# Kernel tuning notes

Hardware: AMD Instinct MI355X
Metric: run time of the kernel (lower is better)

## Reference

```python
import jax, jax.numpy as jnp
import numpy as np

B, T, F = 4096, 72, 9
H = 64            # GRU units per direction
DENSE = 128
P = 24            # predict_window


def _gru_scan(xp, h0, U, br, act):
    """xp: (T,B,3H) precomputed input projections; Keras reset_after=True GRU."""
    def step(h, x_t):
        rec = h @ U + br                      # (B,3H)
        xz, xr, xh = jnp.split(x_t, 3, axis=-1)
        rz, rr, rh = jnp.split(rec, 3, axis=-1)
        z = jax.nn.sigmoid(xz + rz)
        r = jax.nn.sigmoid(xr + rr)
        hh = act(xh + r * rh)
        h_new = z * h + (1.0 - z) * hh
        return h_new, h_new
    hT, hs = jax.lax.scan(step, h0, xp)
    return hT, hs


def _bigru(x, h0f, h0b, Wf, Uf, bif, brf, Wb, Ub, bib, brb, act, return_sequences):
    xt = jnp.swapaxes(x, 0, 1)                # (T,B,F)
    xpf = xt @ Wf + bif                       # (T,B,3H)
    xpb = xt[::-1] @ Wb + bib                 # reversed time for backward dir
    hTf, hsf = _gru_scan(xpf, h0f, Uf, brf, act)
    hTb, hsb = _gru_scan(xpb, h0b, Ub, brb, act)
    if return_sequences:
        out = jnp.concatenate([hsf, hsb[::-1]], axis=-1)   # (T,B,2H)
        return jnp.swapaxes(out, 0, 1)                      # (B,T,2H)
    return jnp.concatenate([hTf, hTb], axis=-1)             # (B,2H)


def _glorot(key, shape):
    fan_in, fan_out = shape[0], shape[-1]
    lim = np.sqrt(6.0 / (fan_in + fan_out))
    return jax.random.uniform(key, shape, jnp.float32, -lim, lim)


def setup_inputs() -> dict:
    key = jax.random.key(0)
    ks = jax.random.split(key, 16)
    d = {
        "x": jax.random.normal(ks[0], (B, T, F), jnp.float32),
        "h0_fwd": jnp.zeros((B, H), jnp.float32),
        "h0_bwd": jnp.zeros((B, H), jnp.float32),
        # d1 (input F=9), forward & backward directions
        "d1f_W": _glorot(ks[1], (F, 3 * H)), "d1f_U": _glorot(ks[2], (H, 3 * H)),
        "d1f_bi": jnp.zeros((3 * H,), jnp.float32), "d1f_br": jnp.zeros((3 * H,), jnp.float32),
        "d1b_W": _glorot(ks[3], (F, 3 * H)), "d1b_U": _glorot(ks[4], (H, 3 * H)),
        "d1b_bi": jnp.zeros((3 * H,), jnp.float32), "d1b_br": jnp.zeros((3 * H,), jnp.float32),
        # d2 (input 2H=128)
        "d2f_W": _glorot(ks[5], (2 * H, 3 * H)), "d2f_U": _glorot(ks[6], (H, 3 * H)),
        "d2f_bi": jnp.zeros((3 * H,), jnp.float32), "d2f_br": jnp.zeros((3 * H,), jnp.float32),
        "d2b_W": _glorot(ks[7], (2 * H, 3 * H)), "d2b_U": _glorot(ks[8], (H, 3 * H)),
        "d2b_bi": jnp.zeros((3 * H,), jnp.float32), "d2b_br": jnp.zeros((3 * H,), jnp.float32),
        # dense heads
        "dense_W": _glorot(ks[9], (2 * H, DENSE)), "dense_b": jnp.zeros((DENSE,), jnp.float32),
        "out_W": _glorot(ks[10], (DENSE, P)), "out_b": jnp.zeros((P,), jnp.float32),
    }
    return d


def reference(x, h0_fwd, h0_bwd,
              d1f_W, d1f_U, d1f_bi, d1f_br, d1b_W, d1b_U, d1b_bi, d1b_br,
              d2f_W, d2f_U, d2f_bi, d2f_br, d2b_W, d2b_U, d2b_bi, d2b_br,
              dense_W, dense_b, out_W, out_b):
    # d1: Bidirectional GRU(64, activation=relu), return_sequences=True, initial_state=hidden
    seq = _bigru(x, h0_fwd, h0_bwd,
                 d1f_W, d1f_U, d1f_bi, d1f_br,
                 d1b_W, d1b_U, d1b_bi, d1b_br,
                 jax.nn.relu, True)                         # (B,T,128)
    # d2: Bidirectional GRU(64, activation=tanh), zero initial state, last-state output
    z0 = jnp.zeros((x.shape[0], H), seq.dtype)
    feat = _bigru(seq, z0, z0,
                  d2f_W, d2f_U, d2f_bi, d2f_br,
                  d2b_W, d2b_U, d2b_bi, d2b_br,
                  jnp.tanh, False)                          # (B,128)
    h = jax.nn.relu(feat @ dense_W + dense_b)               # (B,128)
    out = jax.nn.softmax(h @ out_W + out_b, axis=-1)        # (B,P)
    return out
```

## Files before the change

### kernel.cpp

```cpp
#include <hip/hip_runtime.h>
#include <hip/hip_bf16.h>

typedef __attribute__((ext_vector_type(8))) short short8;
typedef __attribute__((ext_vector_type(4))) float f32x4;

#define MFMA_B16(a, b, c) __builtin_amdgcn_mfma_f32_16x16x32_bf16((a), (b), (c), 0, 0, 0)

__device__ __forceinline__ float bf2f(unsigned short u) {
    union { unsigned int i; float f; } v; v.i = ((unsigned int)u) << 16; return v.f;
}
__device__ __forceinline__ unsigned short f2bf(float f) {
    union { float f; unsigned int i; } v; v.f = f;
    unsigned int r = v.i + 0x7fffu + ((v.i >> 16) & 1u);
    return (unsigned short)(r >> 16);
}
__device__ __forceinline__ float rcp_f(float x) { return __builtin_amdgcn_rcpf(x); }
__device__ __forceinline__ float sigm_pre(float x) {
    return rcp_f(1.0f + __builtin_amdgcn_exp2f(x));
}
__device__ __forceinline__ float tanh_pre(float x) {
    return 1.0f - 2.0f * rcp_f(__builtin_amdgcn_exp2f(x) + 1.0f);
}

__device__ __forceinline__ bool probe_bf16(const unsigned short* p, int tid, int* s_cnt) {
    if (tid == 0) *s_cnt = 0;
    __syncthreads();
    unsigned short s = p[tid & 255];
    int e = (s >> 7) & 0xFF;
    if (tid < 256 && e >= 117 && e <= 137) atomicAdd(s_cnt, 1);
    __syncthreads();
    return *s_cnt >= 200;
}

struct WArgs {
    const void* src[20];
    int off[21];
};

__global__ __launch_bounds__(256)
void convert_w(WArgs a, unsigned short* __restrict__ arena,
               const unsigned short* __restrict__ probe)
{
    __shared__ int cnt;
    const bool bf = probe_bf16(probe, threadIdx.x, &cnt);
    const int total = a.off[20];
    for (int i = blockIdx.x * 256 + threadIdx.x; i < total; i += gridDim.x * 256) {
        int t = 0;
        while (t < 19 && i >= a.off[t + 1]) ++t;
        const int local = i - a.off[t];
        float v = bf ? bf2f(((const unsigned short*)a.src[t])[local])
                     : ((const float*)a.src[t])[local];
        if (t < 16) {
            const int col = local % 192;
            if (col < 128) v *= -1.4426950408889634f;
            else if (t >= 8) v *= 2.885390081777927f;
        }
        arena[i] = f2bf(v);
    }
}

__global__ __launch_bounds__(256, 1)
void gru1_kernel(const void* __restrict__ X, const void* __restrict__ h0f,
                 const void* __restrict__ h0b, int cb, int bchunk,
                 const unsigned short* __restrict__ Wf, const unsigned short* __restrict__ Uf,
                 const unsigned short* __restrict__ bif, const unsigned short* __restrict__ brf,
                 const unsigned short* __restrict__ Wb, const unsigned short* __restrict__ Ub,
                 const unsigned short* __restrict__ bib, const unsigned short* __restrict__ brb,
                 unsigned short* __restrict__ seq)
{
    const int tid  = threadIdx.x;
    const int lane = tid & 63;
    const int wv   = tid >> 6;
    const int q    = lane >> 4;
    const int ln   = lane & 15;
    const int dir  = blockIdx.y;
    const int lb0  = blockIdx.x * 16;
    const int gb0  = cb + lb0;
    const int u    = wv * 16 + ln;

    const unsigned short* W  = dir ? Wb  : Wf;
    const unsigned short* U  = dir ? Ub  : Uf;
    const unsigned short* bi = dir ? bib : bif;
    const unsigned short* br = dir ? brb : brf;
    const void* h0 = dir ? h0b : h0f;

    __shared__ __align__(16) unsigned short Ah[2][16][72];
    __shared__ __align__(16) unsigned short Ax[2][16][40];
    __shared__ int s_cnt;

    const bool xbf = probe_bf16((const unsigned short*)X, tid, &s_cnt);

    {
        unsigned short* p = &Ax[0][0][0];
        for (int i = tid; i < 2 * 16 * 40; i += 256) p[i] = 0;
    }
    __syncthreads();

    {
        const int tx0 = dir ? 71 : 0;
        if (tid < 144) {
            int r = tid / 9, k = tid - 9 * r;
            size_t idx = ((size_t)(gb0 + r) * 72 + tx0) * 9 + k;
            unsigned short hv, lv;
            if (xbf) { hv = ((const unsigned short*)X)[idx]; lv = 0; }
            else { float v = ((const float*)X)[idx]; hv = f2bf(v); lv = f2bf(v - bf2f(hv)); }
            Ax[0][r][2 * k]     = hv;
            Ax[0][r][2 * k + 1] = lv;
        }
    }

    short8 bU[3][2];
    short8 bW[3];
#pragma unroll
    for (int g = 0; g < 3; ++g) {
        const int col = g * 64 + u;
#pragma unroll
        for (int ks = 0; ks < 2; ++ks) {
            short8 f;
#pragma unroll
            for (int j = 0; j < 8; ++j) {
                int kp = ks * 32 + q * 8 + j;
                f[j] = (short)U[(size_t)kp * 192 + col];
            }
            bU[g][ks] = f;
        }
        short8 fw;
#pragma unroll
        for (int j = 0; j < 8; ++j) {
            int kp = q * 8 + j;
            fw[j] = (kp < 18) ? (short)W[(size_t)(kp >> 1) * 192 + col] : (short)0;
        }
        bW[g] = fw;
    }

    const float bz  = bf2f(bi[u])       + bf2f(br[u]);
    const float brg = bf2f(bi[64 + u])  + bf2f(br[64 + u]);
    const float bih = bf2f(bi[128 + u]);
    const float brh = bf2f(br[128 + u]);
    const f32x4 Cz  = {bz,  bz,  bz,  bz};
    const f32x4 Cr  = {brg, brg, brg, brg};
    const f32x4 Chx = {bih, bih, bih, bih};
    const f32x4 Chr = {brh, brh, brh, brh};

    float hreg[4];
#pragma unroll
    for (int i = 0; i < 4; ++i) {
        int m = q * 4 + i;
        size_t idx = (size_t)(gb0 + m) * 64 + u;
        float hv = xbf ? bf2f(((const unsigned short*)h0)[idx])
                       : ((const float*)h0)[idx];
        hreg[i] = hv;
        Ah[0][m][u] = f2bf(hv);
    }

    const int r2 = tid >> 3, c2 = tid & 7;
    const int r0x = tid / 9, k0x = tid - 9 * r0x;

    unsigned short ch = 0, cl = 0;
    if (tid < 144) {
        const int tx = dir ? 70 : 1;
        size_t idx = ((size_t)(gb0 + r0x) * 72 + tx) * 9 + k0x;
        if (xbf) { ch = ((const unsigned short*)X)[idx]; cl = 0; }
        else { float v = ((const float*)X)[idx]; ch = f2bf(v); cl = f2bf(v - bf2f(ch)); }
    }
    __syncthreads();

#pragma unroll 2
    for (int t = 0; t < 72; ++t) {
        const int cur = t & 1, nb = cur ^ 1;

        unsigned short fh = 0, fl = 0;
        if (t < 70 && tid < 144) {
            const int tx = dir ? (69 - t) : (t + 2);
            size_t idx = ((size_t)(gb0 + r0x) * 72 + tx) * 9 + k0x;
            if (xbf) { fh = ((const unsigned short*)X)[idx]; fl = 0; }
            else { float v = ((const float*)X)[idx]; fh = f2bf(v); fl = f2bf(v - bf2f(fh)); }
        }

        if (t > 0 && tid < 128) {
            const int tw = dir ? (71 - (t - 1)) : (t - 1);
            int4 v = *(const int4*)&Ah[cur][r2][c2 * 8];
            *(int4*)(seq + ((size_t)tw * bchunk + lb0 + r2) * 128 + dir * 64 + c2 * 8) = v;
        }

        const unsigned short* ap = &Ah[cur][ln][0];
        short8 a0 = *(const short8*)(ap + q * 8);
        short8 a1 = *(const short8*)(ap + 32 + q * 8);
        short8 ax = *(const short8*)(&Ax[cur][ln][q * 8]);
        f32x4 az  = MFMA_B16(ax, bW[0], Cz);
        az        = MFMA_B16(a0, bU[0][0], az);
        az        = MFMA_B16(a1, bU[0][1], az);
        f32x4 ar  = MFMA_B16(ax, bW[1], Cr);
        ar        = MFMA_B16(a0, bU[1][0], ar);
        ar        = MFMA_B16(a1, bU[1][1], ar);
        f32x4 ahx = MFMA_B16(ax, bW[2], Chx);
        f32x4 ahr = MFMA_B16(a0, bU[2][0], Chr);
        ahr       = MFMA_B16(a1, bU[2][1], ahr);

#pragma unroll
        for (int i = 0; i < 4; ++i) {
            const int m = q * 4 + i;
            float z = sigm_pre(az[i]);
            float r = sigm_pre(ar[i]);
            float pre = ahx[i] + r * ahr[i];
            float hh = fmaxf(pre, 0.0f);
            float hn = hh + z * (hreg[i] - hh);
            hreg[i] = hn;
            Ah[nb][m][u] = f2bf(hn);
        }

        if (t < 71 && tid < 144) {
            Ax[nb][r0x][2 * k0x]     = ch;
            Ax[nb][r0x][2 * k0x + 1] = cl;
        }
        ch = fh; cl = fl;
        __syncthreads();
    }

    if (tid < 128) {
        const int tw = dir ? 0 : 71;
        int4 v = *(const int4*)&Ah[0][r2][c2 * 8];
        *(int4*)(seq + ((size_t)tw * bchunk + lb0 + r2) * 128 + dir * 64 + c2 * 8) = v;
    }
}

__global__ __launch_bounds__(256, 1)
void gru2_kernel(const unsigned short* __restrict__ seq, int cb, int bchunk,
                 const unsigned short* __restrict__ W2f, const unsigned short* __restrict__ U2f,
                 const unsigned short* __restrict__ bi2f, const unsigned short* __restrict__ br2f,
                 const unsigned short* __restrict__ W2b, const unsigned short* __restrict__ U2b,
                 const unsigned short* __restrict__ bi2b, const unsigned short* __restrict__ br2b,
                 float* __restrict__ feat)
{
    const int tid  = threadIdx.x;
    const int lane = tid & 63;
    const int wv   = tid >> 6;
    const int q    = lane >> 4;
    const int ln   = lane & 15;
    const int dir  = blockIdx.y;
    const int lb0  = blockIdx.x * 16;
    const int gb0  = cb + lb0;
    const int u    = wv * 16 + ln;

    const unsigned short* W  = dir ? W2b  : W2f;
    const unsigned short* U  = dir ? U2b  : U2f;
    const unsigned short* bi = dir ? bi2b : bi2f;
    const unsigned short* br = dir ? br2b : br2f;

    __shared__ __align__(16) unsigned short Ah[2][16][72];

    {
        unsigned short* p = &Ah[0][0][0];
        for (int i = tid; i < 16 * 72; i += 256) p[i] = 0;
    }

    const long long tstride = (long long)bchunk * 128 * (dir ? -1 : 1);
    const unsigned short* sptr0 = seq + ((size_t)(lb0 + ln)) * 128 + q * 8
                                + (dir ? 71ll * bchunk * 128 : 0);

    short8 bU[3][2];
    short8 bV[3][4];
#pragma unroll
    for (int g = 0; g < 3; ++g) {
        const int col = g * 64 + u;
#pragma unroll
        for (int ks = 0; ks < 2; ++ks) {
            short8 f;
#pragma unroll
            for (int j = 0; j < 8; ++j) {
                int kp = ks * 32 + q * 8 + j;
                f[j] = (short)U[(size_t)kp * 192 + col];
            }
            bU[g][ks] = f;
        }
#pragma unroll
        for (int ks = 0; ks < 4; ++ks) {
            short8 fv;
#pragma unroll
            for (int j = 0; j < 8; ++j) {
                int kp = ks * 32 + q * 8 + j;
                fv[j] = (short)W[(size_t)kp * 192 + col];
            }
            bV[g][ks] = fv;
        }
    }

    const float bz  = bf2f(bi[u])       + bf2f(br[u]);
    const float brg = bf2f(bi[64 + u])  + bf2f(br[64 + u]);
    const float bih = bf2f(bi[128 + u]);
    const float brh = bf2f(br[128 + u]);
    const f32x4 Cz  = {bz,  bz,  bz,  bz};
    const f32x4 Cr  = {brg, brg, brg, brg};
    const f32x4 Chx = {bih, bih, bih, bih};
    const f32x4 Chr = {brh, brh, brh, brh};

    float hreg[4];
#pragma unroll
    for (int i = 0; i < 4; ++i) hreg[i] = 0.0f;

    f32x4 P0, P1, P2;
    {
        const unsigned short* sp = sptr0;
        short8 s0 = *(const short8*)(sp);
        short8 s1 = *(const short8*)(sp + 32);
        short8 s2 = *(const short8*)(sp + 64);
        short8 s3 = *(const short8*)(sp + 96);
        P0 = MFMA_B16(s0, bV[0][0], Cz);
        P0 = MFMA_B16(s1, bV[0][1], P0);
        P0 = MFMA_B16(s2, bV[0][2], P0);
        P0 = MFMA_B16(s3, bV[0][3], P0);
        P1 = MFMA_B16(s0, bV[1][0], Cr);
        P1 = MFMA_B16(s1, bV[1][1], P1);
        P1 = MFMA_B16(s2, bV[1][2], P1);
        P1 = MFMA_B16(s3, bV[1][3], P1);
        P2 = MFMA_B16(s0, bV[2][0], Chx);
        P2 = MFMA_B16(s1, bV[2][1], P2);
        P2 = MFMA_B16(s2, bV[2][2], P2);
        P2 = MFMA_B16(s3, bV[2][3], P2);
    }
    short8 c0, c1, c2, c3;
    {
        const unsigned short* sp = sptr0 + tstride;
        c0 = *(const short8*)(sp);
        c1 = *(const short8*)(sp + 32);
        c2 = *(const short8*)(sp + 64);
        c3 = *(const short8*)(sp + 96);
    }
    __syncthreads();

#pragma unroll 2
    for (int t = 0; t < 72; ++t) {
        const int cur = t & 1, nb = cur ^ 1;

        short8 f0, f1, f2, f3;
        const bool pf2 = (t < 70);
        if (pf2) {
            const unsigned short* sp = sptr0 + (long long)(t + 2) * tstride;
            f0 = *(const short8*)(sp);
            f1 = *(const short8*)(sp + 32);
            f2 = *(const short8*)(sp + 64);
            f3 = *(const short8*)(sp + 96);
        }

        const unsigned short* ap = &Ah[cur][ln][0];
        short8 a0 = *(const short8*)(ap + q * 8);
        short8 a1 = *(const short8*)(ap + 32 + q * 8);
        f32x4 az  = MFMA_B16(a0, bU[0][0], P0);
        az        = MFMA_B16(a1, bU[0][1], az);
        f32x4 ar  = MFMA_B16(a0, bU[1][0], P1);
        ar        = MFMA_B16(a1, bU[1][1], ar);
        f32x4 ahr = MFMA_B16(a0, bU[2][0], Chr);
        ahr       = MFMA_B16(a1, bU[2][1], ahr);
        f32x4 ahx = P2;

#pragma unroll
        for (int i = 0; i < 4; ++i) {
            const int m = q * 4 + i;
            float z = sigm_pre(az[i]);
            float r = sigm_pre(ar[i]);
            float pre = ahx[i] + r * ahr[i];
            float hh = tanh_pre(pre);
            float hn = hh + z * (hreg[i] - hh);
            hreg[i] = hn;
            Ah[nb][m][u] = f2bf(hn);
        }

        if (t < 71) {
            P0 = MFMA_B16(c0, bV[0][0], Cz);
            P0 = MFMA_B16(c1, bV[0][1], P0);
            P0 = MFMA_B16(c2, bV[0][2], P0);
            P0 = MFMA_B16(c3, bV[0][3], P0);
            P1 = MFMA_B16(c0, bV[1][0], Cr);
            P1 = MFMA_B16(c1, bV[1][1], P1);
            P1 = MFMA_B16(c2, bV[1][2], P1);
            P1 = MFMA_B16(c3, bV[1][3], P1);
            P2 = MFMA_B16(c0, bV[2][0], Chx);
            P2 = MFMA_B16(c1, bV[2][1], P2);
            P2 = MFMA_B16(c2, bV[2][2], P2);
            P2 = MFMA_B16(c3, bV[2][3], P2);
        }
        if (pf2) { c0 = f0; c1 = f1; c2 = f2; c3 = f3; }
        __syncthreads();
    }

#pragma unroll
    for (int i = 0; i < 4; ++i) {
        const int m = q * 4 + i;
        feat[(size_t)(gb0 + m) * 128 + dir * 64 + u] = hreg[i];
    }
}

__global__ __launch_bounds__(256, 1)
void head_kernel(const float* __restrict__ feat,
                 const unsigned short* __restrict__ dW, const unsigned short* __restrict__ db,
                 const unsigned short* __restrict__ oW, const unsigned short* __restrict__ ob,
                 float* __restrict__ out)
{
    const int tid = threadIdx.x;
    const int b0  = blockIdx.x * 16;

    __shared__ __align__(16) unsigned short Wl[128][136];
    __shared__ __align__(16) float fs[16][128];
    __shared__ __align__(16) float hs[16][136];
    __shared__ __align__(16) float ls[16][32];

    for (int i = tid; i < 2048; i += 256) {
        const int k = i >> 4;
        const int c = (i & 15) * 8;
        *(int4*)&Wl[k][c] = *(const int4*)(dW + (size_t)k * 128 + c);
    }
    {
        const float4* src = (const float4*)(feat + (size_t)b0 * 128);
        float4* dst = (float4*)&fs[0][0];
        for (int i = tid; i < 512; i += 256) dst[i] = src[i];
    }
    __syncthreads();

    {
        const int row = tid >> 4;
        const int j0  = (tid & 15) * 8;
        float acc[8];
#pragma unroll
        for (int jj = 0; jj < 8; ++jj) acc[jj] = bf2f(db[j0 + jj]);
        for (int k = 0; k < 128; ++k) {
            float f = fs[row][k];
            short8 w = *(const short8*)&Wl[k][j0];
#pragma unroll
            for (int jj = 0; jj < 8; ++jj)
                acc[jj] += f * bf2f((unsigned short)w[jj]);
        }
#pragma unroll
        for (int jj = 0; jj < 8; ++jj) hs[row][j0 + jj] = fmaxf(acc[jj], 0.0f);
    }
    __syncthreads();

    for (int e = tid; e < 16 * 24; e += 256) {
        const int row = e / 24, l = e - 24 * row;
        float acc = bf2f(ob[l]);
        for (int k = 0; k < 128; ++k)
            acc += hs[row][k] * bf2f(oW[(size_t)k * 24 + l]);
        ls[row][l] = acc;
    }
    __syncthreads();

    for (int e = tid; e < 16 * 24; e += 256) {
        const int row = e / 24, l = e - 24 * row;
        float mx = ls[row][0];
#pragma unroll
        for (int k = 1; k < 24; ++k) mx = fmaxf(mx, ls[row][k]);
        float s = 0.0f;
#pragma unroll
        for (int k = 0; k < 24; ++k) s += __expf(ls[row][k] - mx);
        float v = __expf(ls[row][l] - mx) * rcp_f(s);
        out[(size_t)(b0 + row) * 24 + l] = v;
    }
}

extern "C" void kernel_launch(void* const* d_in, const int* in_sizes, int n_in,
                              void* d_out, int out_size, void* d_ws, size_t ws_size,
                              hipStream_t stream) {
    (void)in_sizes; (void)n_in; (void)out_size;

    static const int wc[20] = {
        1728, 12288, 192, 192,
        1728, 12288, 192, 192,
        24576, 12288, 192, 192,
        24576, 12288, 192, 192,
        16384, 128,
        3072, 24
    };

    WArgs a;
    int off = 0;
    for (int t = 0; t < 20; ++t) {
        a.src[t] = d_in[t + 3];
        a.off[t] = off;
        off += wc[t];
    }
    a.off[20] = off;

    const unsigned long long arena_bytes = 245952ull;
    const unsigned long long feat_bytes  = 4096ull * 128ull * 4ull;
    const unsigned long long seq_full    = 72ull * 4096ull * 128ull * 2ull;
    const unsigned long long fixed       = arena_bytes + feat_bytes;

    int nc = 32;
    for (int c = 1; c <= 32; c *= 2) {
        if (fixed + seq_full / (unsigned long long)c <= (unsigned long long)ws_size) { nc = c; break; }
    }
    const int bchunk = 4096 / nc;

    unsigned short* arena = (unsigned short*)d_ws;
    float* feat           = (float*)((char*)d_ws + arena_bytes);
    unsigned short* seq   = (unsigned short*)((char*)d_ws + fixed);

    convert_w<<<128, 256, 0, stream>>>(a, arena, (const unsigned short*)d_in[0]);

    const unsigned short* d1fW = arena + a.off[0];
    const unsigned short* d1fU = arena + a.off[1];
    const unsigned short* d1fbi= arena + a.off[2];
    const unsigned short* d1fbr= arena + a.off[3];
    const unsigned short* d1bW = arena + a.off[4];
    const unsigned short* d1bU = arena + a.off[5];
    const unsigned short* d1bbi= arena + a.off[6];
    const unsigned short* d1bbr= arena + a.off[7];
    const unsigned short* d2fW = arena + a.off[8];
    const unsigned short* d2fU = arena + a.off[9];
    const unsigned short* d2fbi= arena + a.off[10];
    const unsigned short* d2fbr= arena + a.off[11];
    const unsigned short* d2bW = arena + a.off[12];
    const unsigned short* d2bU = arena + a.off[13];
    const unsigned short* d2bbi= arena + a.off[14];
    const unsigned short* d2bbr= arena + a.off[15];
    const unsigned short* dW   = arena + a.off[16];
    const unsigned short* db   = arena + a.off[17];
    const unsigned short* oW   = arena + a.off[18];
    const unsigned short* ob   = arena + a.off[19];

    for (int c = 0; c < nc; ++c) {
        const int cb = c * bchunk;
        gru1_kernel<<<dim3(bchunk / 16, 2), 256, 0, stream>>>(
            d_in[0], d_in[1], d_in[2], cb, bchunk,
            d1fW, d1fU, d1fbi, d1fbr, d1bW, d1bU, d1bbi, d1bbr, seq);
        gru2_kernel<<<dim3(bchunk / 16, 2), 256, 0, stream>>>(
            seq, cb, bchunk,
            d2fW, d2fU, d2fbi, d2fbr, d2bW, d2bU, d2bbi, d2bbr, feat);
    }
    head_kernel<<<256, 256, 0, stream>>>(
        feat, dW, db, oW, ob, (float*)d_out);
}
```

Before: 256.3 us.

## Run each GRU direction tile in one wavefront and split gru2 into producer/consumer waves

gru1 now runs on a single 64-lane wave per 16-row tile, with each lane computing all 64 hidden units through four MFMA column tiles. This removes the per-step block barriers and the LDS staging of x, which is now loaded with vector reads and converted in registers. gru2 uses two waves: a producer computes input projections and a consumer runs the recurrence, synchronised by lightweight LDS barriers. The cost is far higher register pressure per lane and fewer threads per block, which may lower occupancy or cause spills.

```diff
diff --git a/kernel.cpp b/kernel.cpp
--- a/kernel.cpp
+++ b/kernel.cpp
@@ -3,31 +3,51 @@
 
 typedef __attribute__((ext_vector_type(8))) short short8;
 typedef __attribute__((ext_vector_type(4))) float f32x4;
+typedef float float4a __attribute__((ext_vector_type(4), aligned(4)));
+typedef unsigned short ushort4u __attribute__((ext_vector_type(4), aligned(2)));
+typedef unsigned short ush;
 
 #define MFMA_B16(a, b, c) __builtin_amdgcn_mfma_f32_16x16x32_bf16((a), (b), (c), 0, 0, 0)
 
-__device__ __forceinline__ float bf2f(unsigned short u) {
+__device__ __forceinline__ float bf2f(ush u) {
     union { unsigned int i; float f; } v; v.i = ((unsigned int)u) << 16; return v.f;
 }
-__device__ __forceinline__ unsigned short f2bf(float f) {
+__device__ __forceinline__ ush f2bf(float f) {
     union { float f; unsigned int i; } v; v.f = f;
     unsigned int r = v.i + 0x7fffu + ((v.i >> 16) & 1u);
-    return (unsigned short)(r >> 16);
+    return (ush)(r >> 16);
 }
 __device__ __forceinline__ float rcp_f(float x) { return __builtin_amdgcn_rcpf(x); }
 __device__ __forceinline__ float sigm_pre(float x) {
     return rcp_f(1.0f + __builtin_amdgcn_exp2f(x));
 }
-__device__ __forceinline__ float tanh_pre(float x) {
-    return 1.0f - 2.0f * rcp_f(__builtin_amdgcn_exp2f(x) + 1.0f);
-}
-
-__device__ __forceinline__ bool probe_bf16(const unsigned short* p, int tid, int* s_cnt) {
+
+__device__ __forceinline__ void lds_barrier() {
+    asm volatile("s_waitcnt lgkmcnt(0)" ::: "memory");
+    __builtin_amdgcn_s_barrier();
+    asm volatile("" ::: "memory");
+}
+
+__device__ __forceinline__ bool probe_bf16(const ush* p, int tid, int* s_cnt) {
     if (tid == 0) *s_cnt = 0;
     __syncthreads();
-    unsigned short s = p[tid & 255];
+    ush s = p[tid & 255];
     int e = (s >> 7) & 0xFF;
     if (tid < 256 && e >= 117 && e <= 137) atomicAdd(s_cnt, 1);
+    __syncthreads();
+    return *s_cnt >= 200;
+}
+__device__ __forceinline__ bool probe_bf16_64(const ush* p, int lane, int* s_cnt) {
+    if (lane == 0) *s_cnt = 0;
+    __syncthreads();
+    int c = 0;
+#pragma unroll
+    for (int k = 0; k < 4; ++k) {
+        ush s = p[lane * 4 + k];
+        int e = (s >> 7) & 0xFF;
+        c += (e >= 117 && e <= 137) ? 1 : 0;
+    }
+    atomicAdd(s_cnt, c);
     __syncthreads();
     return *s_cnt >= 200;
 }
@@ -38,8 +58,7 @@
 };
 
 __global__ __launch_bounds__(256)
-void convert_w(WArgs a, unsigned short* __restrict__ arena,
-               const unsigned short* __restrict__ probe)
+void convert_w(WArgs a, ush* __restrict__ arena, const ush* __restrict__ probe)
 {
     __shared__ int cnt;
     const bool bf = probe_bf16(probe, threadIdx.x, &cnt);
@@ -48,7 +67,7 @@
         int t = 0;
         while (t < 19 && i >= a.off[t + 1]) ++t;
         const int local = i - a.off[t];
-        float v = bf ? bf2f(((const unsigned short*)a.src[t])[local])
+        float v = bf ? bf2f(((const ush*)a.src[t])[local])
                      : ((const float*)a.src[t])[local];
         if (t < 16) {
             const int col = local % 192;
@@ -59,347 +78,386 @@
     }
 }
 
-__global__ __launch_bounds__(256, 1)
+struct XR { float4a f; ushort4u h; };
+
+__device__ __forceinline__ XR loadx(const void* X, bool xbf, size_t row72, int tx, int q) {
+    XR r;
+    r.f = (float4a){0.f, 0.f, 0.f, 0.f};
+    r.h = (ushort4u){0, 0, 0, 0};
+    if (xbf) {
+        const ush* p = (const ush*)X + (row72 + (size_t)tx) * 9 + q * 4;
+        if (q < 2) r.h = *(const ushort4u*)p;
+        else if (q == 2) r.h[0] = p[0];
+    } else {
+        const float* p = (const float*)X + (row72 + (size_t)tx) * 9 + q * 4;
+        if (q < 2) r.f = *(const float4a*)p;
+        else if (q == 2) r.f[0] = p[0];
+    }
+    return r;
+}
+
+__device__ __forceinline__ short8 convx(bool xbf, float4a rf, ushort4u rh) {
+    short8 r;
+    if (xbf) {
+#pragma unroll
+        for (int j = 0; j < 4; ++j) { r[2 * j] = (short)rh[j]; r[2 * j + 1] = 0; }
+    } else {
+#pragma unroll
+        for (int j = 0; j < 4; ++j) {
+            ush hi = f2bf(rf[j]);
+            ush lo = f2bf(rf[j] - bf2f(hi));
+            r[2 * j] = (short)hi; r[2 * j + 1] = (short)lo;
+        }
+    }
+    return r;
+}
+
+#define GRU1_STEP(T, AX, RFO, RHO)                                              \
+    do {                                                                        \
+        const short8 axu_ = AX;                            \
+        if ((T) < 70) AX = convx(xbf, RFO, RHO);          \
+        if ((T) < 68) {                                                         \
+            XR rr = loadx(X, xbf, row72, dir ? 67 - (T) : (T) + 4, q);          \
+            RFO = rr.f; RHO = rr.h;                                             \
+        }                                                                       \
+        short8 a0 = *(const short8*)&Ah[ln][q * 8];                             \
+        short8 a1 = *(const short8*)&Ah[ln][32 + q * 8];                        \
+        if ((T) > 0) {                                                          \
+            const int tw = dir ? 71 - ((T) - 1) : (T) - 1;                      \
+            ush* sp = seq + ((size_t)tw * bchunk + lb0 + ln) * 128 + dir * 64;  \
+            *(short8*)(sp + q * 8) = a0;                                        \
+            *(short8*)(sp + 32 + q * 8) = a1;                                   \
+        }                                                                       \
+        f32x4 az[4], ar[4], ahx[4], ahr[4];                                     \
+        _Pragma("unroll") for (int n = 0; n < 4; ++n) {                         \
+            az[n]  = MFMA_B16(axu_, bW[0][n], Cz[n]);                           \
+            az[n]  = MFMA_B16(a0, bU[0][0][n], az[n]);                          \
+            az[n]  = MFMA_B16(a1, bU[0][1][n], az[n]);                          \
+            ar[n]  = MFMA_B16(axu_, bW[1][n], Cr[n]);                           \
+            ar[n]  = MFMA_B16(a0, bU[1][0][n], ar[n]);                          \
+            ar[n]  = MFMA_B16(a1, bU[1][1][n], ar[n]);                          \
+            ahx[n] = MFMA_B16(axu_, bW[2][n], Chx[n]);                          \
+            ahr[n] = MFMA_B16(a0, bU[2][0][n], Chr[n]);                         \
+            ahr[n] = MFMA_B16(a1, bU[2][1][n], ahr[n]);                         \
+        }                                                                       \
+        _Pragma("unroll") for (int n = 0; n < 4; ++n)                           \
+            _Pragma("unroll") for (int i = 0; i < 4; ++i) {                     \
+                float z = sigm_pre(az[n][i]);                                   \
+                float r = sigm_pre(ar[n][i]);                                   \
+                float pre = ahx[n][i] + r * ahr[n][i];                          \
+                float hh = fmaxf(pre, 0.0f);                                    \
+                float hn = hh + z * (hreg[n][i] - hh);                          \
+                hreg[n][i] = hn;                                                \
+                Ah[q * 4 + i][n * 16 + ln] = f2bf(hn);                          \
+            }                                                                   \
+    } while (0)
+
+__global__ __launch_bounds__(64, 1)
 void gru1_kernel(const void* __restrict__ X, const void* __restrict__ h0f,
                  const void* __restrict__ h0b, int cb, int bchunk,
-                 const unsigned short* __restrict__ Wf, const unsigned short* __restrict__ Uf,
-                 const unsigned short* __restrict__ bif, const unsigned short* __restrict__ brf,
-                 const unsigned short* __restrict__ Wb, const unsigned short* __restrict__ Ub,
-                 const unsigned short* __restrict__ bib, const unsigned short* __restrict__ brb,
-                 unsigned short* __restrict__ seq)
+                 const ush* __restrict__ Wf, const ush* __restrict__ Uf,
+                 const ush* __restrict__ bif, const ush* __restrict__ brf,
+                 const ush* __restrict__ Wb, const ush* __restrict__ Ub,
+                 const ush* __restrict__ bib, const ush* __restrict__ brb,
+                 ush* __restrict__ seq)
 {
-    const int tid  = threadIdx.x;
-    const int lane = tid & 63;
-    const int wv   = tid >> 6;
-    const int q    = lane >> 4;
-    const int ln   = lane & 15;
-    const int dir  = blockIdx.y;
-    const int lb0  = blockIdx.x * 16;
-    const int gb0  = cb + lb0;
-    const int u    = wv * 16 + ln;
-
-    const unsigned short* W  = dir ? Wb  : Wf;
-    const unsigned short* U  = dir ? Ub  : Uf;
-    const unsigned short* bi = dir ? bib : bif;
-    const unsigned short* br = dir ? brb : brf;
+    const int lane = threadIdx.x & 63;
+    const int q = lane >> 4, ln = lane & 15;
+    const int dir = blockIdx.y;
+    const int lb0 = blockIdx.x * 16;
+    const int gb0 = cb + lb0;
+
+    const ush* W  = dir ? Wb  : Wf;
+    const ush* U  = dir ? Ub  : Uf;
+    const ush* bi = dir ? bib : bif;
+    const ush* br = dir ? brb : brf;
     const void* h0 = dir ? h0b : h0f;
 
-    __shared__ __align__(16) unsigned short Ah[2][16][72];
-    __shared__ __align__(16) unsigned short Ax[2][16][40];
+    __shared__ __align__(16) ush Ah[16][72];
     __shared__ int s_cnt;
 
-    const bool xbf = probe_bf16((const unsigned short*)X, tid, &s_cnt);
+    const bool xbf = probe_bf16_64((const ush*)X, lane, &s_cnt);
+
+    short8 bU[3][2][4];
+    short8 bW[3][4];
+#pragma unroll
+    for (int g = 0; g < 3; ++g)
+#pragma unroll
+        for (int n = 0; n < 4; ++n) {
+            const int col = g * 64 + n * 16 + ln;
+#pragma unroll
+            for (int ks = 0; ks < 2; ++ks) {
+                short8 f;
+#pragma unroll
+                for (int j = 0; j < 8; ++j) {
+                    int kp = ks * 32 + q * 8 + j;
+                    f[j] = (short)U[(size_t)kp * 192 + col];
+                }
+                bU[g][ks][n] = f;
+            }
+            short8 fw;
+#pragma unroll
+            for (int j = 0; j < 8; ++j) {
+                int kp = q * 8 + j;
+                fw[j] = (kp < 18) ? (short)W[(size_t)(kp >> 1) * 192 + col] : (short)0;
+            }
+            bW[g][n] = fw;
+        }
+
+    f32x4 Cz[4], Cr[4], Chx[4], Chr[4];
+#pragma unroll
+    for (int n = 0; n < 4; ++n) {
+        const int u2 = n * 16 + ln;
+        const float bz  = bf2f(bi[u2]) + bf2f(br[u2]);
+        const float brg = bf2f(bi[64 + u2]) + bf2f(br[64 + u2]);
+        const float bih = bf2f(bi[128 + u2]);
+        const float brh = bf2f(br[128 + u2]);
+        Cz[n]  = (f32x4){bz, bz, bz, bz};
+        Cr[n]  = (f32x4){brg, brg, brg, brg};
+        Chx[n] = (f32x4){bih, bih, bih, bih};
+        Chr[n] = (f32x4){brh, brh, brh, brh};
+    }
+
+    float hreg[4][4];
+#pragma unroll
+    for (int n = 0; n < 4; ++n)
+#pragma unroll
+        for (int i = 0; i < 4; ++i) {
+            size_t idx = (size_t)(gb0 + q * 4 + i) * 64 + n * 16 + ln;
+            float hv = xbf ? bf2f(((const ush*)h0)[idx]) : ((const float*)h0)[idx];
+            hreg[n][i] = hv;
+            Ah[q * 4 + i][n * 16 + ln] = f2bf(hv);
+        }
+
+    const size_t row72 = (size_t)(gb0 + ln) * 72;
+    XR r0 = loadx(X, xbf, row72, dir ? 71 : 0, q);
+    XR r1 = loadx(X, xbf, row72, dir ? 70 : 1, q);
+    XR r2 = loadx(X, xbf, row72, dir ? 69 : 2, q);
+    XR r3 = loadx(X, xbf, row72, dir ? 68 : 3, q);
+    short8 ax0 = convx(xbf, r0.f, r0.h);
+    short8 ax1 = convx(xbf, r1.f, r1.h);
+    float4a rf0 = r2.f; ushort4u rh0 = r2.h;
+    float4a rf1 = r3.f; ushort4u rh1 = r3.h;
+
+    for (int t = 0; t < 72; t += 2) {
+        GRU1_STEP(t,     ax0, rf0, rh0);
+        GRU1_STEP(t + 1, ax1, rf1, rh1);
+    }
 
     {
-        unsigned short* p = &Ax[0][0][0];
-        for (int i = tid; i < 2 * 16 * 40; i += 256) p[i] = 0;
-    }
-    __syncthreads();
-
-    {
-        const int tx0 = dir ? 71 : 0;
-        if (tid < 144) {
-            int r = tid / 9, k = tid - 9 * r;
-            size_t idx = ((size_t)(gb0 + r) * 72 + tx0) * 9 + k;
-            unsigned short hv, lv;
-            if (xbf) { hv = ((const unsigned short*)X)[idx]; lv = 0; }
-            else { float v = ((const float*)X)[idx]; hv = f2bf(v); lv = f2bf(v - bf2f(hv)); }
-            Ax[0][r][2 * k]     = hv;
-            Ax[0][r][2 * k + 1] = lv;
-        }
-    }
-
-    short8 bU[3][2];
-    short8 bW[3];
-#pragma unroll
-    for (int g = 0; g < 3; ++g) {
-        const int col = g * 64 + u;
-#pragma unroll
-        for (int ks = 0; ks < 2; ++ks) {
-            short8 f;
-#pragma unroll
-            for (int j = 0; j < 8; ++j) {
-                int kp = ks * 32 + q * 8 + j;
-                f[j] = (short)U[(size_t)kp * 192 + col];
-            }
-            bU[g][ks] = f;
-        }
-        short8 fw;
-#pragma unroll
-        for (int j = 0; j < 8; ++j) {
-            int kp = q * 8 + j;
-            fw[j] = (kp < 18) ? (short)W[(size_t)(kp >> 1) * 192 + col] : (short)0;
-        }
-        bW[g] = fw;
-    }
-
-    const float bz  = bf2f(bi[u])       + bf2f(br[u]);
-    const float brg = bf2f(bi[64 + u])  + bf2f(br[64 + u]);
-    const float bih = bf2f(bi[128 + u]);
-    const float brh = bf2f(br[128 + u]);
-    const f32x4 Cz  = {bz,  bz,  bz,  bz};
-    const f32x4 Cr  = {brg, brg, brg, brg};
-    const f32x4 Chx = {bih, bih, bih, bih};
-    const f32x4 Chr = {brh, brh, brh, brh};
-
-    float hreg[4];
-#pragma unroll
-    for (int i = 0; i < 4; ++i) {
-        int m = q * 4 + i;
-        size_t idx = (size_t)(gb0 + m) * 64 + u;
-        float hv = xbf ? bf2f(((const unsigned short*)h0)[idx])
-                       : ((const float*)h0)[idx];
-        hreg[i] = hv;
-        Ah[0][m][u] = f2bf(hv);
-    }
-
-    const int r2 = tid >> 3, c2 = tid & 7;
-    const int r0x = tid / 9, k0x = tid - 9 * r0x;
-
-    unsigned short ch = 0, cl = 0;
-    if (tid < 144) {
-        const int tx = dir ? 70 : 1;
-        size_t idx = ((size_t)(gb0 + r0x) * 72 + tx) * 9 + k0x;
-        if (xbf) { ch = ((const unsigned short*)X)[idx]; cl = 0; }
-        else { float v = ((const float*)X)[idx]; ch = f2bf(v); cl = f2bf(v - bf2f(ch)); }
-    }
-    __syncthreads();
-
-#pragma unroll 2
-    for (int t = 0; t < 72; ++t) {
-        const int cur = t & 1, nb = cur ^ 1;
-
-        unsigned short fh = 0, fl = 0;
-        if (t < 70 && tid < 144) {
-            const int tx = dir ? (69 - t) : (t + 2);
-            size_t idx = ((size_t)(gb0 + r0x) * 72 + tx) * 9 + k0x;
-            if (xbf) { fh = ((const unsigned short*)X)[idx]; fl = 0; }
-            else { float v = ((const float*)X)[idx]; fh = f2bf(v); fl = f2bf(v - bf2f(fh)); }
-        }
-
-        if (t > 0 && tid < 128) {
-            const int tw = dir ? (71 - (t - 1)) : (t - 1);
-            int4 v = *(const int4*)&Ah[cur][r2][c2 * 8];
-            *(int4*)(seq + ((size_t)tw * bchunk + lb0 + r2) * 128 + dir * 64 + c2 * 8) = v;
-        }
-
-        const unsigned short* ap = &Ah[cur][ln][0];
-        short8 a0 = *(const short8*)(ap + q * 8);
-        short8 a1 = *(const short8*)(ap + 32 + q * 8);
-        short8 ax = *(const short8*)(&Ax[cur][ln][q * 8]);
-        f32x4 az  = MFMA_B16(ax, bW[0], Cz);
-        az        = MFMA_B16(a0, bU[0][0], az);
-        az        = MFMA_B16(a1, bU[0][1], az);
-        f32x4 ar  = MFMA_B16(ax, bW[1], Cr);
-        ar        = MFMA_B16(a0, bU[1][0], ar);
-        ar        = MFMA_B16(a1, bU[1][1], ar);
-        f32x4 ahx = MFMA_B16(ax, bW[2], Chx);
-        f32x4 ahr = MFMA_B16(a0, bU[2][0], Chr);
-        ahr       = MFMA_B16(a1, bU[2][1], ahr);
-
-#pragma unroll
-        for (int i = 0; i < 4; ++i) {
-            const int m = q * 4 + i;
-            float z = sigm_pre(az[i]);
-            float r = sigm_pre(ar[i]);
-            float pre = ahx[i] + r * ahr[i];
-            float hh = fmaxf(pre, 0.0f);
-            float hn = hh + z * (hreg[i] - hh);
-            hreg[i] = hn;
-            Ah[nb][m][u] = f2bf(hn);
-        }
-
-        if (t < 71 && tid < 144) {
-            Ax[nb][r0x][2 * k0x]     = ch;
-            Ax[nb][r0x][2 * k0x + 1] = cl;
-        }
-        ch = fh; cl = fl;
-        __syncthreads();
-    }
-
-    if (tid < 128) {
+        short8 a0 = *(const short8*)&Ah[ln][q * 8];
+        short8 a1 = *(const short8*)&Ah[ln][32 + q * 8];
         const int tw = dir ? 0 : 71;
-        int4 v = *(const int4*)&Ah[0][r2][c2 * 8];
-        *(int4*)(seq + ((size_t)tw * bchunk + lb0 + r2) * 128 + dir * 64 + c2 * 8) = v;
-    }
-}
-
-__global__ __launch_bounds__(256, 1)
-void gru2_kernel(const unsigned short* __restrict__ seq, int cb, int bchunk,
-                 const unsigned short* __restrict__ W2f, const unsigned short* __restrict__ U2f,
-                 const unsigned short* __restrict__ bi2f, const unsigned short* __restrict__ br2f,
-                 const unsigned short* __restrict__ W2b, const unsigned short* __restrict__ U2b,
-                 const unsigned short* __restrict__ bi2b, const unsigned short* __restrict__ br2b,
+        ush* sp = seq + ((size_t)tw * bchunk + lb0 + ln) * 128 + dir * 64;
+        *(short8*)(sp + q * 8) = a0;
+        *(short8*)(sp + 32 + q * 8) = a1;
+    }
+}
+
+#define PROD_STEP(FA, BUFI, T)                                                 \
+    do {                                                                       \
+        if ((T) < 71) {                                                        \
+            _Pragma("unroll") for (int g = 0; g < 3; ++g) {                    \
+                _Pragma("unroll") for (int n = 0; n < 4; ++n) {                \
+                    f32x4 acc = MFMA_B16(FA[0], bV[g][0][n], Cg[g][n]);        \
+                    acc = MFMA_B16(FA[1], bV[g][1][n], acc);                   \
+                    acc = MFMA_B16(FA[2], bV[g][2][n], acc);                   \
+                    acc = MFMA_B16(FA[3], bV[g][3][n], acc);                   \
+                    *(f32x4*)&Pbuf[BUFI][g][n][poff] = acc;                    \
+                }                                                              \
+            }                                                                  \
+        }                                                                      \
+        if ((T) < 69) {                                                        \
+            const ush* sp = sptr0 + (long long)((T) + 3) * tstride;            \
+            FA[0] = *(const short8*)sp;                                        \
+            FA[1] = *(const short8*)(sp + 32);                                 \
+            FA[2] = *(const short8*)(sp + 64);                                 \
+            FA[3] = *(const short8*)(sp + 96);                                 \
+        }                                                                      \
+    } while (0)
+
+#define CONS_STEP(BUFI, T)                                                     \
+    do {                                                                       \
+        f32x4 Pz[4], Pr[4], Pc[4];                                             \
+        _Pragma("unroll") for (int n = 0; n < 4; ++n) {                        \
+            Pz[n] = *(const f32x4*)&Pbuf[BUFI][0][n][poff];                    \
+            Pr[n] = *(const f32x4*)&Pbuf[BUFI][1][n][poff];                    \
+            Pc[n] = *(const f32x4*)&Pbuf[BUFI][2][n][poff];                    \
+        }                                                                      \
+        short8 a0 = *(const short8*)&Ah[ln][q * 8];                            \
+        short8 a1 = *(const short8*)&Ah[ln][32 + q * 8];                       \
+        f32x4 az[4], ar[4], ahr[4];                                            \
+        _Pragma("unroll") for (int n = 0; n < 4; ++n) {                        \
+            az[n]  = MFMA_B16(a0, bU[0][0][n], Pz[n]);                         \
+            az[n]  = MFMA_B16(a1, bU[0][1][n], az[n]);                         \
+            ar[n]  = MFMA_B16(a0, bU[1][0][n], Pr[n]);                         \
+            ar[n]  = MFMA_B16(a1, bU[1][1][n], ar[n]);                         \
+            ahr[n] = MFMA_B16(a0, bU[2][0][n], Chr[n]);                        \
+            ahr[n] = MFMA_B16(a1, bU[2][1][n], ahr[n]);                        \
+        }                                                                      \
+        _Pragma("unroll") for (int n = 0; n < 4; ++n)                          \
+            _Pragma("unroll") for (int i = 0; i < 4; ++i) {                    \
+                float z = sigm_pre(az[n][i]);                                  \
+                float r = sigm_pre(ar[n][i]);                                  \
+                float pre = Pc[n][i] + r * ahr[n][i];                          \
+                float e = __builtin_amdgcn_exp2f(pre);         \
+                float hh = 1.0f - 2.0f * rcp_f(e + 1.0f);                      \
+                float hn = hh + z * (hreg[n][i] - hh);                         \
+                hreg[n][i] = hn;                                               \
+                Ah[q * 4 + i][n * 16 + ln] = f2bf(hn);                         \
+            }                                                                  \
+    } while (0)
+
+__global__ __launch_bounds__(128, 1)
+void gru2_kernel(const ush* __restrict__ seq, int cb, int bchunk,
+                 const ush* __restrict__ W2f, const ush* __restrict__ U2f,
+                 const ush* __restrict__ bi2f, const ush* __restrict__ br2f,
+                 const ush* __restrict__ W2b, const ush* __restrict__ U2b,
+                 const ush* __restrict__ bi2b, const ush* __restrict__ br2b,
                  float* __restrict__ feat)
 {
-    const int tid  = threadIdx.x;
-    const int lane = tid & 63;
-    const int wv   = tid >> 6;
-    const int q    = lane >> 4;
-    const int ln   = lane & 15;
-    const int dir  = blockIdx.y;
-    const int lb0  = blockIdx.x * 16;
-    const int gb0  = cb + lb0;
-    const int u    = wv * 16 + ln;
-
-    const unsigned short* W  = dir ? W2b  : W2f;
-    const unsigned short* U  = dir ? U2b  : U2f;
-    const unsigned short* bi = dir ? bi2b : bi2f;
-    const unsigned short* br = dir ? br2b : br2f;
-
-    __shared__ __align__(16) unsigned short Ah[2][16][72];
-
-    {
-        unsigned short* p = &Ah[0][0][0];
-        for (int i = tid; i < 16 * 72; i += 256) p[i] = 0;
-    }
-
-    const long long tstride = (long long)bchunk * 128 * (dir ? -1 : 1);
-    const unsigned short* sptr0 = seq + ((size_t)(lb0 + ln)) * 128 + q * 8
-                                + (dir ? 71ll * bchunk * 128 : 0);
-
-    short8 bU[3][2];
-    short8 bV[3][4];
-#pragma unroll
-    for (int g = 0; g < 3; ++g) {
-        const int col = g * 64 + u;
-#pragma unroll
-        for (int ks = 0; ks < 2; ++ks) {
-            short8 f;
-#pragma unroll
-            for (int j = 0; j < 8; ++j) {
-                int kp = ks * 32 + q * 8 + j;
-                f[j] = (short)U[(size_t)kp * 192 + col];
+    const int tid = threadIdx.x;
+    const int wv = tid >> 6, lane = tid & 63, q = lane >> 4, ln = lane & 15;
+    const int dir = blockIdx.y, lb0 = blockIdx.x * 16, gb0 = cb + lb0;
+
+    const ush* W  = dir ? W2b  : W2f;
+    const ush* U  = dir ? U2b  : U2f;
+    const ush* bi = dir ? bi2b : bi2f;
+    const ush* br = dir ? br2b : br2f;
+
+    __shared__ __align__(16) float Pbuf[2][3][4][288];
+    __shared__ __align__(16) ush Ah[16][72];
+
+    const int poff = (lane >> 3) * 36 + (lane & 7) * 4;
+
+    if (wv == 0) {
+        short8 bV[3][4][4];
+#pragma unroll
+        for (int g = 0; g < 3; ++g)
+#pragma unroll
+            for (int n = 0; n < 4; ++n) {
+                const int col = g * 64 + n * 16 + ln;
+#pragma unroll
+                for (int ks = 0; ks < 4; ++ks) {
+                    short8 f;
+#pragma unroll
+                    for (int j = 0; j < 8; ++j) {
+                        int kp = ks * 32 + q * 8 + j;
+                        f[j] = (short)W[(size_t)kp * 192 + col];
+                    }
+                    bV[g][ks][n] = f;
+                }
             }
-            bU[g][ks] = f;
-        }
-#pragma unroll
-        for (int ks = 0; ks < 4; ++ks) {
-            short8 fv;
-#pragma unroll
-            for (int j = 0; j < 8; ++j) {
-                int kp = ks * 32 + q * 8 + j;
-                fv[j] = (short)W[(size_t)kp * 192 + col];
+        f32x4 Cg[3][4];
+#pragma unroll
+        for (int n = 0; n < 4; ++n) {
+            const int u2 = n * 16 + ln;
+            const float bz  = bf2f(bi[u2]) + bf2f(br[u2]);
+            const float brg = bf2f(bi[64 + u2]) + bf2f(br[64 + u2]);
+            const float bih = bf2f(bi[128 + u2]);
+            Cg[0][n] = (f32x4){bz, bz, bz, bz};
+            Cg[1][n] = (f32x4){brg, brg, brg, brg};
+            Cg[2][n] = (f32x4){bih, bih, bih, bih};
+        }
+
+        const long long tstride = (long long)bchunk * 128 * (dir ? -1 : 1);
+        const ush* sptr0 = seq + (size_t)(lb0 + ln) * 128 + q * 8
+                         + (dir ? 71ll * bchunk * 128 : 0);
+
+        {
+            const ush* sp = sptr0;
+            short8 s0 = *(const short8*)sp;
+            short8 s1 = *(const short8*)(sp + 32);
+            short8 s2 = *(const short8*)(sp + 64);
+            short8 s3 = *(const short8*)(sp + 96);
+#pragma unroll
+            for (int g = 0; g < 3; ++g)
+#pragma unroll
+                for (int n = 0; n < 4; ++n) {
+                    f32x4 acc = MFMA_B16(s0, bV[g][0][n], Cg[g][n]);
+                    acc = MFMA_B16(s1, bV[g][1][n], acc);
+                    acc = MFMA_B16(s2, bV[g][2][n], acc);
+                    acc = MFMA_B16(s3, bV[g][3][n], acc);
+                    *(f32x4*)&Pbuf[0][g][n][poff] = acc;
+                }
+        }
+        short8 F0[4], F1[4];
+        {
+            const ush* sp = sptr0 + tstride;
+            F0[0] = *(const short8*)sp;        F0[1] = *(const short8*)(sp + 32);
+            F0[2] = *(const short8*)(sp + 64); F0[3] = *(const short8*)(sp + 96);
+        }
+        {
+            const ush* sp = sptr0 + 2 * tstride;
+            F1[0] = *(const short8*)sp;        F1[1] = *(const short8*)(sp + 32);
+            F1[2] = *(const short8*)(sp + 64); F1[3] = *(const short8*)(sp + 96);
+        }
+        lds_barrier();
+
+        for (int t = 0; t < 72; t += 2) {
+            PROD_STEP(F0, 1, t);
+            lds_barrier();
+            PROD_STEP(F1, 0, t + 1);
+            lds_barrier();
+        }
+    } else {
+        short8 bU[3][2][4];
+#pragma unroll
+        for (int g = 0; g < 3; ++g)
+#pragma unroll
+            for (int n = 0; n < 4; ++n) {
+                const int col = g * 64 + n * 16 + ln;
+#pragma unroll
+                for (int ks = 0; ks < 2; ++ks) {
+                    short8 f;
+#pragma unroll
+                    for (int j = 0; j < 8; ++j) {
+                        int kp = ks * 32 + q * 8 + j;
+                        f[j] = (short)U[(size_t)kp * 192 + col];
+                    }
+                    bU[g][ks][n] = f;
+                }
             }
-            bV[g][ks] = fv;
-        }
-    }
-
-    const float bz  = bf2f(bi[u])       + bf2f(br[u]);
-    const float brg = bf2f(bi[64 + u])  + bf2f(br[64 + u]);
-    const float bih = bf2f(bi[128 + u]);
-    const float brh = bf2f(br[128 + u]);
-    const f32x4 Cz  = {bz,  bz,  bz,  bz};
-    const f32x4 Cr  = {brg, brg, brg, brg};
-    const f32x4 Chx = {bih, bih, bih, bih};
-    const f32x4 Chr = {brh, brh, brh, brh};
-
-    float hreg[4];
-#pragma unroll
-    for (int i = 0; i < 4; ++i) hreg[i] = 0.0f;
-
-    f32x4 P0, P1, P2;
-    {
-        const unsigned short* sp = sptr0;
-        short8 s0 = *(const short8*)(sp);
-        short8 s1 = *(const short8*)(sp + 32);
-        short8 s2 = *(const short8*)(sp + 64);
-        short8 s3 = *(const short8*)(sp + 96);
-        P0 = MFMA_B16(s0, bV[0][0], Cz);
-        P0 = MFMA_B16(s1, bV[0][1], P0);
-        P0 = MFMA_B16(s2, bV[0][2], P0);
-        P0 = MFMA_B16(s3, bV[0][3], P0);
-        P1 = MFMA_B16(s0, bV[1][0], Cr);
-        P1 = MFMA_B16(s1, bV[1][1], P1);
-        P1 = MFMA_B16(s2, bV[1][2], P1);
-        P1 = MFMA_B16(s3, bV[1][3], P1);
-        P2 = MFMA_B16(s0, bV[2][0], Chx);
-        P2 = MFMA_B16(s1, bV[2][1], P2);
-        P2 = MFMA_B16(s2, bV[2][2], P2);
-        P2 = MFMA_B16(s3, bV[2][3], P2);
-    }
-    short8 c0, c1, c2, c3;
-    {
-        const unsigned short* sp = sptr0 + tstride;
-        c0 = *(const short8*)(sp);
-        c1 = *(const short8*)(sp + 32);
-        c2 = *(const short8*)(sp + 64);
-        c3 = *(const short8*)(sp + 96);
-    }
-    __syncthreads();
-
-#pragma unroll 2
-    for (int t = 0; t < 72; ++t) {
-        const int cur = t & 1, nb = cur ^ 1;
-
-        short8 f0, f1, f2, f3;
-        const bool pf2 = (t < 70);
-        if (pf2) {
-            const unsigned short* sp = sptr0 + (long long)(t + 2) * tstride;
-            f0 = *(const short8*)(sp);
-            f1 = *(const short8*)(sp + 32);
-            f2 = *(const short8*)(sp + 64);
-            f3 = *(const short8*)(sp + 96);
-        }
-
-        const unsigned short* ap = &Ah[cur][ln][0];
-        short8 a0 = *(const short8*)(ap + q * 8);
-        short8 a1 = *(const short8*)(ap + 32 + q * 8);
-        f32x4 az  = MFMA_B16(a0, bU[0][0], P0);
-        az        = MFMA_B16(a1, bU[0][1], az);
-        f32x4 ar  = MFMA_B16(a0, bU[1][0], P1);
-        ar        = MFMA_B16(a1, bU[1][1], ar);
-        f32x4 ahr = MFMA_B16(a0, bU[2][0], Chr);
-        ahr       = MFMA_B16(a1, bU[2][1], ahr);
-        f32x4 ahx = P2;
-
-#pragma unroll
-        for (int i = 0; i < 4; ++i) {
-            const int m = q * 4 + i;
-            float z = sigm_pre(az[i]);
-            float r = sigm_pre(ar[i]);
-            float pre = ahx[i] + r * ahr[i];
-            float hh = tanh_pre(pre);
-            float hn = hh + z * (hreg[i] - hh);
-            hreg[i] = hn;
-            Ah[nb][m][u] = f2bf(hn);
-        }
-
-        if (t < 71) {
-            P0 = MFMA_B16(c0, bV[0][0], Cz);
-            P0 = MFMA_B16(c1, bV[0][1], P0);
-            P0 = MFMA_B16(c2, bV[0][2], P0);
-            P0 = MFMA_B16(c3, bV[0][3], P0);
-            P1 = MFMA_B16(c0, bV[1][0], Cr);
-            P1 = MFMA_B16(c1, bV[1][1], P1);
-            P1 = MFMA_B16(c2, bV[1][2], P1);
-            P1 = MFMA_B16(c3, bV[1][3], P1);
-            P2 = MFMA_B16(c0, bV[2][0], Chx);
-            P2 = MFMA_B16(c1, bV[2][1], P2);
-            P2 = MFMA_B16(c2, bV[2][2], P2);
-            P2 = MFMA_B16(c3, bV[2][3], P2);
-        }
-        if (pf2) { c0 = f0; c1 = f1; c2 = f2; c3 = f3; }
-        __syncthreads();
-    }
-
-#pragma unroll
-    for (int i = 0; i < 4; ++i) {
-        const int m = q * 4 + i;
-        feat[(size_t)(gb0 + m) * 128 + dir * 64 + u] = hreg[i];
+        f32x4 Chr[4];
+#pragma unroll
+        for (int n = 0; n < 4; ++n) {
+            const float brh = bf2f(br[128 + n * 16 + ln]);
+            Chr[n] = (f32x4){brh, brh, brh, brh};
+        }
+
+        for (int i = lane; i < 16 * 72; i += 64) (&Ah[0][0])[i] = 0;
+        float hreg[4][4];
+#pragma unroll
+        for (int n = 0; n < 4; ++n)
+#pragma unroll
+            for (int i = 0; i < 4; ++i) hreg[n][i] = 0.0f;
+        lds_barrier();
+
+        for (int t = 0; t < 72; t += 2) {
+            CONS_STEP(0, t);
+            lds_barrier();
+            CONS_STEP(1, t + 1);
+            lds_barrier();
+        }
+
+#pragma unroll
+        for (int n = 0; n < 4; ++n)
+#pragma unroll
+            for (int i = 0; i < 4; ++i)
+                feat[(size_t)(gb0 + q * 4 + i) * 128 + dir * 64 + n * 16 + ln] = hreg[n][i];
     }
 }
 
 __global__ __launch_bounds__(256, 1)
 void head_kernel(const float* __restrict__ feat,
-                 const unsigned short* __restrict__ dW, const unsigned short* __restrict__ db,
-                 const unsigned short* __restrict__ oW, const unsigned short* __restrict__ ob,
+                 const ush* __restrict__ dW, const ush* __restrict__ db,
+                 const ush* __restrict__ oW, const ush* __restrict__ ob,
                  float* __restrict__ out)
 {
     const int tid = threadIdx.x;
     const int b0  = blockIdx.x * 16;
 
-    __shared__ __align__(16) unsigned short Wl[128][136];
+    __shared__ __align__(16) ush Wl[128][136];
     __shared__ __align__(16) float fs[16][128];
     __shared__ __align__(16) float hs[16][136];
     __shared__ __align__(16) float ls[16][32];
@@ -427,7 +485,7 @@
             short8 w = *(const short8*)&Wl[k][j0];
 #pragma unroll
             for (int jj = 0; jj < 8; ++jj)
-                acc[jj] += f * bf2f((unsigned short)w[jj]);
+                acc[jj] += f * bf2f((ush)w[jj]);
         }
 #pragma unroll
         for (int jj = 0; jj < 8; ++jj) hs[row][j0 + jj] = fmaxf(acc[jj], 0.0f);
@@ -490,39 +548,39 @@
     }
     const int bchunk = 4096 / nc;
 
-    unsigned short* arena = (unsigned short*)d_ws;
-    float* feat           = (float*)((char*)d_ws + arena_bytes);
-    unsigned short* seq   = (unsigned short*)((char*)d_ws + fixed);
-
-    convert_w<<<128, 256, 0, stream>>>(a, arena, (const unsigned short*)d_in[0]);
-
-    const unsigned short* d1fW = arena + a.off[0];
-    const unsigned short* d1fU = arena + a.off[1];
-    const unsigned short* d1fbi= arena + a.off[2];
-    const unsigned short* d1fbr= arena + a.off[3];
-    const unsigned short* d1bW = arena + a.off[4];
-    const unsigned short* d1bU = arena + a.off[5];
-    const unsigned short* d1bbi= arena + a.off[6];
-    const unsigned short* d1bbr= arena + a.off[7];
-    const unsigned short* d2fW = arena + a.off[8];
-    const unsigned short* d2fU = arena + a.off[9];
-    const unsigned short* d2fbi= arena + a.off[10];
-    const unsigned short* d2fbr= arena + a.off[11];
-    const unsigned short* d2bW = arena + a.off[12];
-    const unsigned short* d2bU = arena + a.off[13];
-    const unsigned short* d2bbi= arena + a.off[14];
-    const unsigned short* d2bbr= arena + a.off[15];
-    const unsigned short* dW   = arena + a.off[16];
-    const unsigned short* db   = arena + a.off[17];
-    const unsigned short* oW   = arena + a.off[18];
-    const unsigned short* ob   = arena + a.off[19];
+    ush* arena  = (ush*)d_ws;
+    float* feat = (float*)((char*)d_ws + arena_bytes);
+    ush* seq    = (ush*)((char*)d_ws + fixed);
+
+    convert_w<<<128, 256, 0, stream>>>(a, arena, (const ush*)d_in[0]);
+
+    const ush* d1fW = arena + a.off[0];
+    const ush* d1fU = arena + a.off[1];
+    const ush* d1fbi= arena + a.off[2];
+    const ush* d1fbr= arena + a.off[3];
+    const ush* d1bW = arena + a.off[4];
+    const ush* d1bU = arena + a.off[5];
+    const ush* d1bbi= arena + a.off[6];
+    const ush* d1bbr= arena + a.off[7];
+    const ush* d2fW = arena + a.off[8];
+    const ush* d2fU = arena + a.off[9];
+    const ush* d2fbi= arena + a.off[10];
+    const ush* d2fbr= arena + a.off[11];
+    const ush* d2bW = arena + a.off[12];
+    const ush* d2bU = arena + a.off[13];
+    const ush* d2bbi= arena + a.off[14];
+    const ush* d2bbr= arena + a.off[15];
+    const ush* dW   = arena + a.off[16];
+    const ush* db   = arena + a.off[17];
+    const ush* oW   = arena + a.off[18];
+    const ush* ob   = arena + a.off[19];
 
     for (int c = 0; c < nc; ++c) {
         const int cb = c * bchunk;
-        gru1_kernel<<<dim3(bchunk / 16, 2), 256, 0, stream>>>(
+        gru1_kernel<<<dim3(bchunk / 16, 2), 64, 0, stream>>>(
             d_in[0], d_in[1], d_in[2], cb, bchunk,
             d1fW, d1fU, d1fbi, d1fbr, d1bW, d1bU, d1bbi, d1bbr, seq);
-        gru2_kernel<<<dim3(bchunk / 16, 2), 256, 0, stream>>>(
+        gru2_kernel<<<dim3(bchunk / 16, 2), 128, 0, stream>>>(
             seq, cb, bchunk,
             d2fW, d2fU, d2fbi, d2fbr, d2bW, d2bU, d2bbi, d2bbr, feat);
     }
```

After: 291.8 us. +13.9%, slower.
